# Optimization experiments

Measured on AMD Instinct MI355X. Metric: run time of the kernel, lower is better.

## Reference

```python
import jax, jax.numpy as jnp
import numpy as np

B0, H0, W0 = 4, 64, 64
D_MODEL, D_STATE, D_CONV, EXPAND = 192, 16, 3, 2.0
D_INNER = int(EXPAND * D_MODEL)          # 384
DT_RANK = (D_MODEL + 1) // 2             # 96
K = 4
EPS = 1e-5


def setup_inputs() -> dict:
    key = jax.random.key(0)
    ks = jax.random.split(key, 10)
    x = jax.random.normal(ks[0], (B0, H0, W0, D_MODEL), dtype=jnp.float32)
    in_proj_w = jax.random.normal(ks[1], (2 * D_INNER, D_MODEL), jnp.float32) * (D_MODEL ** -0.5)
    conv_w = jax.random.normal(ks[2], (D_INNER, 1, D_CONV, D_CONV), jnp.float32) * (1.0 / D_CONV)
    conv_b = jnp.zeros((D_INNER,), jnp.float32)
    x_proj_weight = jax.random.normal(ks[3], (K, DT_RANK + 2 * D_STATE, D_INNER), jnp.float32) * (D_INNER ** -0.5)
    dt_init_std = DT_RANK ** -0.5
    dt_projs_weight = jax.random.uniform(ks[4], (K, D_INNER, DT_RANK), jnp.float32, -dt_init_std, dt_init_std)
    # inverse-softplus init of dt bias, dt ~ loguniform[1e-3, 0.1]
    u = jax.random.uniform(ks[5], (K, D_INNER), jnp.float32)
    dt = jnp.exp(u * (np.log(0.1) - np.log(0.001)) + np.log(0.001))
    dt = jnp.clip(dt, 1e-4, None)
    dt_projs_bias = dt + jnp.log(-jnp.expm1(-dt))
    A_logs = jnp.log(jnp.tile(jnp.arange(1, D_STATE + 1, dtype=jnp.float32)[None, :], (K * D_INNER, 1)))
    Ds = jnp.ones((K * D_INNER,), jnp.float32)
    ln_gamma = jnp.ones((D_INNER,), jnp.float32)
    ln_beta = jnp.zeros((D_INNER,), jnp.float32)
    out_proj_w = jax.random.normal(ks[6], (D_MODEL, D_INNER), jnp.float32) * (D_INNER ** -0.5)
    return dict(x=x, in_proj_w=in_proj_w, conv_w=conv_w, conv_b=conv_b,
                x_proj_weight=x_proj_weight, dt_projs_weight=dt_projs_weight,
                dt_projs_bias=dt_projs_bias, A_logs=A_logs, Ds=Ds,
                ln_gamma=ln_gamma, ln_beta=ln_beta, out_proj_w=out_proj_w)


def _selective_scan(u, delta, A, Bs, Cs, Dp):
    # u, delta: (B,K,D,L); A: (K,D,N); Bs, Cs: (B,K,N,L); Dp: (K,D)
    b = u.shape[0]
    uT = jnp.transpose(u, (3, 0, 1, 2))      # (L,B,K,D)
    dT = jnp.transpose(delta, (3, 0, 1, 2))  # (L,B,K,D)
    BT = jnp.transpose(Bs, (3, 0, 1, 2))     # (L,B,K,N)
    CT = jnp.transpose(Cs, (3, 0, 1, 2))     # (L,B,K,N)
    h0 = jnp.zeros((b, K, D_INNER, D_STATE), u.dtype)

    def step(h, inp):
        dl, ul, Bl, Cl = inp
        dA = jnp.exp(dl[..., None] * A)                      # (B,K,D,N)
        h = dA * h + (dl * ul)[..., None] * Bl[:, :, None, :]  # (B,K,D,N)
        y = jnp.einsum('bkdn,bkn->bkd', h, Cl)
        return h, y

    _, ys = jax.lax.scan(step, h0, (dT, uT, BT, CT))
    y = jnp.transpose(ys, (1, 2, 3, 0))       # (B,K,D,L)
    return y + u * Dp[None, :, :, None]


def reference(x, in_proj_w, conv_w, conv_b, x_proj_weight, dt_projs_weight,
              dt_projs_bias, A_logs, Ds, ln_gamma, ln_beta, out_proj_w):
    B, H, W, C = x.shape
    L = H * W
    xz = jnp.einsum('bhwc,dc->bhwd', x, in_proj_w)           # (B,H,W,2*Di)
    xp, z = jnp.split(xz, 2, axis=-1)
    xc = jnp.transpose(xp, (0, 3, 1, 2))                      # (B,Di,H,W)
    xc = jax.lax.conv_general_dilated(
        xc, conv_w, window_strides=(1, 1), padding='SAME',
        feature_group_count=D_INNER,
        dimension_numbers=('NCHW', 'OIHW', 'NCHW')) + conv_b[None, :, None, None]
    xc = jax.nn.silu(xc)

    # cross-scan: 4 traversal orders
    x_flat = xc.reshape(B, D_INNER, L)
    x_wh = jnp.transpose(xc, (0, 1, 3, 2)).reshape(B, D_INNER, L)
    x_hwwh = jnp.stack([x_flat, x_wh], axis=1)                # (B,2,Di,L)
    xs = jnp.concatenate([x_hwwh, jnp.flip(x_hwwh, axis=-1)], axis=1)  # (B,4,Di,L)

    x_dbl = jnp.einsum('bkdl,kcd->bkcl', xs, x_proj_weight)
    dts = x_dbl[:, :, :DT_RANK]
    Bs = x_dbl[:, :, DT_RANK:DT_RANK + D_STATE]
    Cs = x_dbl[:, :, DT_RANK + D_STATE:]
    dts = jnp.einsum('bkrl,kdr->bkdl', dts, dt_projs_weight)
    delta = jax.nn.softplus(dts + dt_projs_bias[None, :, :, None])

    A = -jnp.exp(A_logs).reshape(K, D_INNER, D_STATE)
    Dp = Ds.reshape(K, D_INNER)
    out_y = _selective_scan(xs, delta, A, Bs, Cs, Dp)         # (B,4,Di,L)

    y1 = out_y[:, 0]
    inv_y = jnp.flip(out_y[:, 2:4], axis=-1)
    y2 = inv_y[:, 0]
    y3 = jnp.transpose(out_y[:, 1].reshape(B, D_INNER, W, H), (0, 1, 3, 2)).reshape(B, D_INNER, L)
    y4 = jnp.transpose(inv_y[:, 1].reshape(B, D_INNER, W, H), (0, 1, 3, 2)).reshape(B, D_INNER, L)
    y = y1 + y2 + y3 + y4                                     # (B,Di,L)

    y = jnp.transpose(y, (0, 2, 1)).reshape(B, H, W, D_INNER)
    mu = jnp.mean(y, axis=-1, keepdims=True)
    var = jnp.mean(jnp.square(y - mu), axis=-1, keepdims=True)
    y = (y - mu) * jax.lax.rsqrt(var + EPS) * ln_gamma + ln_beta
    y = y * jax.nn.silu(z)
    return jnp.einsum('bhwd,cd->bhwc', y, out_proj_w)
```

## Files before the change

kernel.cpp:

```cpp
#include <hip/hip_runtime.h>
#include <cstdint>

#define NSTATE  16
#define NCH     128
#define CH      32

typedef short bf16x8 __attribute__((ext_vector_type(8)));
typedef float f32x4  __attribute__((ext_vector_type(4)));
typedef float f32x2  __attribute__((ext_vector_type(2)));

__device__ __forceinline__ float b2f(unsigned short u) {
    union { unsigned int i; float f; } v; v.i = ((unsigned int)u) << 16; return v.f;
}
__device__ __forceinline__ unsigned short f2b(float f) {
    union { float f; unsigned int i; } v; v.f = f;
    unsigned int r = v.i + 0x7FFFu + ((v.i >> 16) & 1u);
    return (unsigned short)(r >> 16);
}
__device__ __forceinline__ f32x2 b2f2(unsigned int w) {
    union { unsigned int i; float f; } lo, hi;
    lo.i = w << 16; hi.i = w & 0xFFFF0000u;
    f32x2 r; r.x = lo.f; r.y = hi.f; return r;
}
__device__ __forceinline__ unsigned int f2b2(f32x2 v) {
    return (unsigned int)f2b(v.x) | ((unsigned int)f2b(v.y) << 16);
}
__device__ __forceinline__ f32x2 fma2(f32x2 a, f32x2 b, f32x2 c) {
#if __has_builtin(__builtin_elementwise_fma)
    return __builtin_elementwise_fma(a, b, c);
#else
    f32x2 r; r.x = fmaf(a.x, b.x, c.x); r.y = fmaf(a.y, b.y, c.y); return r;
#endif
}
__device__ __forceinline__ float exp2_fast(float x) {
    return __builtin_amdgcn_exp2f(x);
}
__device__ __forceinline__ float softplus_fast(float v) {
    return fmaxf(v, 0.f) + __logf(1.f + __expf(-fabsf(v)));
}
__device__ __forceinline__ void gload16(const void* g, void* l) {
    __builtin_amdgcn_global_load_lds(
        (const __attribute__((address_space(1))) void*)g,
        (__attribute__((address_space(3))) void*)l, 16, 0, 0);
}

__device__ __forceinline__ int pmap(int k, int i) {
    int l = i;
    if (k & 2) l = 4095 - l;
    if (k & 1) l = ((l & 63) << 6) | (l >> 6);
    return l;
}

__device__ __forceinline__ void epowers2(f32x2 E, f32x2* a) {
    a[0] = E;
    a[1] = a[0] * a[0];
    a[2] = a[1] * a[0];
    a[3] = a[1] * a[1];
    a[4] = a[3] * a[0];
    a[5] = a[3] * a[1];
    a[6] = a[3] * a[2];
    a[7] = a[3] * a[3];
    a[8]  = a[7] * a[0];
    a[9]  = a[7] * a[1];
    a[10] = a[7] * a[2];
    a[11] = a[7] * a[3];
    a[12] = a[7] * a[4];
    a[13] = a[7] * a[5];
    a[14] = a[7] * a[6];
    a[15] = a[7] * a[7];
}

__global__ __launch_bounds__(256)
void cast5(const float* __restrict__ s0, const float* __restrict__ s1,
           const float* __restrict__ s2, const float* __restrict__ s3,
           const float* __restrict__ s4, unsigned short* __restrict__ dst,
           int o1, int o2, int o3, int o4, int total)
{
    int i = (blockIdx.x * 256 + threadIdx.x) * 4;
    if (i >= total) return;
    const float* s; int off;
    if (i < o1)      { s = s0; off = 0;  }
    else if (i < o2) { s = s1; off = o1; }
    else if (i < o3) { s = s2; off = o2; }
    else if (i < o4) { s = s3; off = o3; }
    else             { s = s4; off = o4; }
    float4 v = *(const float4*)(s + (i - off));
    unsigned short o[4] = { f2b(v.x), f2b(v.y), f2b(v.z), f2b(v.w) };
    *(uint2*)(dst + i) = *(const uint2*)o;
}

__global__ __launch_bounds__(384)
void weff_k(const float* __restrict__ dtw, const float* __restrict__ xpw,
            unsigned short* __restrict__ wallb)
{
    int k = blockIdx.x;
    int dblk = blockIdx.y;
    int dp = threadIdx.x;
    if (dblk < 48) {
        const float* xb = xpw + (size_t)k * 128 * 384;
        const float* db = dtw + ((size_t)k * 384 + dblk * 8) * 96;
        float acc[8];
#pragma unroll
        for (int j = 0; j < 8; ++j) acc[j] = 0.f;
        for (int r = 0; r < 96; ++r) {
            float xv = xb[(size_t)r * 384 + dp];
#pragma unroll
            for (int j = 0; j < 8; ++j) acc[j] = fmaf(db[(size_t)j * 96 + r], xv, acc[j]);
        }
#pragma unroll
        for (int j = 0; j < 8; ++j)
            wallb[((size_t)k * 512 + dblk * 8 + j) * 384 + dp] = f2b(acc[j]);
    } else if (dblk < 52) {
        int r0 = (dblk - 48) * 8;
#pragma unroll
        for (int j = 0; j < 8; ++j)
            wallb[((size_t)k * 512 + 384 + r0 + j) * 384 + dp] =
                f2b(xpw[((size_t)k * 128 + 96 + r0 + j) * 384 + dp]);
    } else {
        int r0 = 416 + (dblk - 52) * 8;
#pragma unroll
        for (int j = 0; j < 8; ++j)
            wallb[((size_t)k * 512 + r0 + j) * 384 + dp] = 0;
    }
}

template<int MAP, int EPI, int OUTBF>
__global__ __launch_bounds__(512)
void gemm_pk3(const unsigned short* __restrict__ A, const unsigned short* __restrict__ A2,
              const unsigned short* __restrict__ W, void* __restrict__ Cv,
              float* __restrict__ aux, const float* __restrict__ bias,
              int Kd, int lda, int ldc, int wstride)
{
    __shared__ unsigned short As[3 * 256 * 32];
    __shared__ unsigned short Ws[3 * 128 * 32];
    const int bm = blockIdx.y * 256;
    const int bn = blockIdx.x * 128;
    const int t = threadIdx.x;
    const int lane = t & 63;
    const int wv = t >> 6;
    const int wm = wv & 3;
    const int wn = wv >> 2;

    int kb = 0;
    if (wstride) kb = (bm >> 12) & 3;
    const unsigned short* Wb = W + (size_t)kb * wstride;

    f32x4 acc[4][4];
#pragma unroll
    for (int i = 0; i < 4; ++i)
#pragma unroll
        for (int j = 0; j < 4; ++j) acc[i][j] = (f32x4){0.f, 0.f, 0.f, 0.f};

    const int cs = (t & 3) ^ ((t >> 3) & 3);
    const unsigned short* agsrc[2];
#pragma unroll
    for (int j = 0; j < 2; ++j) {
        int chunk = j * 512 + t;
        int row = chunk >> 2;
        size_t ro;
        if (MAP == 0) {
            ro = (size_t)(bm + row) * lda;
        } else {
            int r = bm + row;
            int bk = r >> 12, ii = r & 4095;
            int k = bk & 3, b = bk >> 2;
            int l = (k & 2) ? 4095 - ii : ii;
            const unsigned short* src = (k & 1) ? A2 : A;
            ro = (src - A) + ((size_t)b * 4096 + l) * 384;
        }
        agsrc[j] = A + ro + cs * 8;
    }
    const unsigned short* wgsrc = Wb + (size_t)(bn + (t >> 2)) * Kd + cs * 8;

    const int lr = lane & 15;
    const int chq = ((lane >> 4) ^ ((lane >> 1) & 3)) * 8;
    const int NT = Kd >> 5;

    auto stage = [&](int kt2, int buf) {
        const int k0 = kt2 << 5;
        char* asb = (char*)As + buf * 16384 + wv * 1024;
        char* wsb = (char*)Ws + buf * 8192 + wv * 1024;
        gload16(agsrc[0] + k0, asb);
        gload16(agsrc[1] + k0, asb + 8192);
        gload16(wgsrc + k0, wsb);
    };

    stage(0, 0);
    stage(1, 1);

    for (int kt = 0; kt < NT; ++kt) {
        if (kt == NT - 1) {
            asm volatile("s_waitcnt vmcnt(0)" ::: "memory");
        } else {
            asm volatile("s_waitcnt vmcnt(3)" ::: "memory");
        }
        __builtin_amdgcn_sched_barrier(0);
        __builtin_amdgcn_s_barrier();
        __builtin_amdgcn_sched_barrier(0);
        if (kt + 2 < NT) stage(kt + 2, (kt + 2) % 3);

        const unsigned short* Ab = As + (kt % 3) * (256 * 32);
        const unsigned short* Wt = Ws + (kt % 3) * (128 * 32);
        bf16x8 af[4], bfr[4];
#pragma unroll
        for (int mf = 0; mf < 4; ++mf)
            af[mf] = *(const bf16x8*)&Ab[(wm * 64 + mf * 16 + lr) * 32 + chq];
#pragma unroll
        for (int nf = 0; nf < 4; ++nf)
            bfr[nf] = *(const bf16x8*)&Wt[(wn * 64 + nf * 16 + lr) * 32 + chq];
#pragma unroll
        for (int mf = 0; mf < 4; ++mf)
#pragma unroll
            for (int nf = 0; nf < 4; ++nf)
                acc[mf][nf] = __builtin_amdgcn_mfma_f32_16x16x32_bf16(af[mf], bfr[nf], acc[mf][nf], 0, 0, 0);
    }

    const int lq = lane >> 4;
#pragma unroll
    for (int mf = 0; mf < 4; ++mf) {
#pragma unroll
        for (int nf = 0; nf < 4; ++nf) {
#pragma unroll
            for (int r = 0; r < 4; ++r) {
                int grow = bm + wm * 64 + mf * 16 + lq * 4 + r;
                int gcol = bn + wn * 64 + nf * 16 + lr;
                float v = acc[mf][nf][r];
                if (EPI == 0) {
                    if (OUTBF) ((unsigned short*)Cv)[(size_t)grow * ldc + gcol] = f2b(v);
                    else       ((float*)Cv)[(size_t)grow * ldc + gcol] = v;
                } else {
                    unsigned cc = (unsigned)gcol;
                    if (cc < 384u) {
                        v += bias[kb * 384 + cc];
                        v = softplus_fast(v);
                        ((unsigned short*)Cv)[(size_t)grow * 384 + cc] = f2b(v);
                    } else if (cc < 416u) {
                        aux[(size_t)grow * 32 + (cc - 384u)] = v;
                    }
                }
            }
        }
    }
}

__global__ __launch_bounds__(384)
void conv_silu(const unsigned short* __restrict__ xzb, const float* __restrict__ cw,
               const float* __restrict__ cb, unsigned short* __restrict__ xcb,
               unsigned short* __restrict__ xcbT)
{
    int t = threadIdx.x;
    int sub = (t >= 192) ? 1 : 0;
    int dp = t - sub * 192;
    int d0 = dp * 2;
    int bidx = blockIdx.x * 2 + sub;
    int l = bidx & 4095;
    int h = l >> 6, w = l & 63;
    const unsigned short* base = xzb + (size_t)(bidx - l) * 768;
    f32x2 acc; acc.x = cb[d0]; acc.y = cb[d0 + 1];
#pragma unroll
    for (int dy = -1; dy <= 1; ++dy) {
        int hh = h + dy;
        if ((unsigned)hh >= 64u) continue;
#pragma unroll
        for (int dx = -1; dx <= 1; ++dx) {
            int ww = w + dx;
            if ((unsigned)ww >= 64u) continue;
            f32x2 xv = b2f2(*(const unsigned int*)&base[(size_t)(hh * 64 + ww) * 768 + d0]);
            int wi = (dy + 1) * 3 + (dx + 1);
            f32x2 wv2; wv2.x = cw[d0 * 9 + wi]; wv2.y = cw[(d0 + 1) * 9 + wi];
            acc = fma2(xv, wv2, acc);
        }
    }
    f32x2 sig;
    sig.x = 1.f / (1.f + __expf(-acc.x));
    sig.y = 1.f / (1.f + __expf(-acc.y));
    acc *= sig;
    unsigned int v = f2b2(acc);
    *(unsigned int*)&xcb[(size_t)bidx * 384 + d0] = v;
    *(unsigned int*)&xcbT[((size_t)(bidx - l) + (w * 64 + h)) * 384 + d0] = v;
}

__global__ __launch_bounds__(384)
void scan1(const unsigned short* __restrict__ delta, const unsigned short* __restrict__ xcb,
           const unsigned short* __restrict__ xcbT, const float* __restrict__ bcf,
           const float* __restrict__ A_logs, unsigned short* __restrict__ csth,
           float* __restrict__ csts)
{
    int bid = blockIdx.x;
    int cpair = bid & 63;
    int bk = bid >> 6;
    int k = bk & 3, b = bk >> 2;
    int t = threadIdx.x;
    int sub = (__builtin_amdgcn_readfirstlane(t) >= 192) ? 1 : 0;
    int dp = t - sub * 192;
    int d0 = dp * 2;
    int c = cpair * 2 + sub;
    int i0 = c * CH;

    f32x2 A0l2;
    A0l2.x = -__expf(A_logs[((size_t)(k * 384 + d0)) * 16]) * 1.44269504f;
    A0l2.y = -__expf(A_logs[((size_t)(k * 384 + d0 + 1)) * 16]) * 1.44269504f;

    f32x2 h[NSTATE];
#pragma unroll
    for (int n = 0; n < NSTATE; ++n) h[n] = (f32x2){0.f, 0.f};
    f32x2 S = (f32x2){0.f, 0.f};

    const float* bcp = bcf + ((size_t)bk * 4096 + i0) * 32;
    size_t drow = ((size_t)bk * 4096 + i0) * 384 + d0;
    const unsigned short* usrc = (k & 1) ? xcbT : xcb;
    long ustep = (k & 2) ? -384 : 384;
    size_t urow = ((size_t)b * 4096 + ((k & 2) ? 4095 - i0 : i0)) * 384 + d0;

    unsigned int dw = *(const unsigned int*)&delta[drow];
    unsigned int uw = *(const unsigned int*)&usrc[urow];

    for (int ii = 0; ii < CH; ++ii) {
        unsigned int dwn = 0, uwn = 0;
        if (ii + 1 < CH) {
            dwn = *(const unsigned int*)&delta[drow + (ii + 1) * 384];
            uwn = *(const unsigned int*)&usrc[urow + (long)(ii + 1) * ustep];
        }
        const f32x4* P = (const f32x4*)(bcp + ii * 32);
        f32x4 B0 = P[0], B1 = P[1], B2 = P[2], B3 = P[3];

        f32x2 dl = b2f2(dw), u = b2f2(uw);
        S += dl;
        f32x2 ex = dl * A0l2;
        f32x2 E; E.x = exp2_fast(ex.x); E.y = exp2_fast(ex.y);
        f32x2 du = dl * u;
        f32x2 a[NSTATE];
        epowers2(E, a);
        float Bs[NSTATE] = {B0.x,B0.y,B0.z,B0.w, B1.x,B1.y,B1.z,B1.w,
                            B2.x,B2.y,B2.z,B2.w, B3.x,B3.y,B3.z,B3.w};
#pragma unroll
        for (int n = 0; n < NSTATE; ++n)
            h[n] = fma2(a[n], h[n], du * (f32x2){Bs[n], Bs[n]});
        dw = dwn; uw = uwn;
    }
    size_t hb = ((size_t)(bk * NCH + c) * 16) * 384 + d0;
#pragma unroll
    for (int n = 0; n < NSTATE; ++n)
        *(unsigned int*)&csth[hb + (size_t)n * 384] = f2b2(h[n]);
    *(f32x2*)&csts[(size_t)(bk * NCH + c) * 384 + d0] = S;
}

__global__ __launch_bounds__(384)
void scan2(unsigned short* __restrict__ csth, const float* __restrict__ csts,
           const float* __restrict__ A_logs)
{
    int bk = blockIdx.x, n = blockIdx.y;
    int d = threadIdx.x;
    int k = bk & 3;
    float An = -__expf(A_logs[((size_t)(k * 384 + d)) * 16 + n]);
    float H = 0.f;
    size_t hb0 = ((size_t)(bk * NCH) * 16 + n) * 384 + d;
    size_t sb0 = (size_t)(bk * NCH) * 384 + d;
    float S  = csts[sb0];
    float hF = b2f(csth[hb0]);
    for (int c = 0; c < NCH; ++c) {
        float Sn = 0.f, hFn = 0.f;
        if (c + 1 < NCH) {
            Sn  = csts[sb0 + (size_t)(c + 1) * 384];
            hFn = b2f(csth[hb0 + (size_t)(c + 1) * 16 * 384]);
        }
        csth[hb0 + (size_t)c * 16 * 384] = f2b(H);
        H = __expf(An * S) * H + hF;
        S = Sn; hF = hFn;
    }
}

__global__ __launch_bounds__(384)
void scan3(const unsigned short* __restrict__ delta, const unsigned short* __restrict__ xcb,
           const unsigned short* __restrict__ xcbT, const float* __restrict__ bcf,
           const float* __restrict__ A_logs, const float* __restrict__ Ds,
           const unsigned short* __restrict__ csth, unsigned short* __restrict__ yb)
{
    int bid = blockIdx.x;
    int cpair = bid & 63;
    int bk = bid >> 6;
    int k = bk & 3, b = bk >> 2;
    int t = threadIdx.x;
    int sub = (__builtin_amdgcn_readfirstlane(t) >= 192) ? 1 : 0;
    int dp = t - sub * 192;
    int d0 = dp * 2;
    int c = cpair * 2 + sub;
    int i0 = c * CH;

    f32x2 A0l2;
    A0l2.x = -__expf(A_logs[((size_t)(k * 384 + d0)) * 16]) * 1.44269504f;
    A0l2.y = -__expf(A_logs[((size_t)(k * 384 + d0 + 1)) * 16]) * 1.44269504f;

    f32x2 h[NSTATE];
    size_t hb = ((size_t)(bk * NCH + c) * 16) * 384 + d0;
#pragma unroll
    for (int n = 0; n < NSTATE; ++n)
        h[n] = b2f2(*(const unsigned int*)&csth[hb + (size_t)n * 384]);
    f32x2 Dp; Dp.x = Ds[k * 384 + d0]; Dp.y = Ds[k * 384 + d0 + 1];

    const float* bcp = bcf + ((size_t)bk * 4096 + i0) * 32;
    size_t drow = ((size_t)bk * 4096 + i0) * 384 + d0;
    const unsigned short* usrc = (k & 1) ? xcbT : xcb;
    long ustep = (k & 2) ? -384 : 384;
    size_t urow = ((size_t)b * 4096 + ((k & 2) ? 4095 - i0 : i0)) * 384 + d0;
    long ystep = (long)((k & 1) ? 64 : 1) * ((k & 2) ? -1 : 1) * 384;
    size_t yrow = ((size_t)bk * 4096 + pmap(k, i0)) * 384 + d0;

    unsigned int dw = *(const unsigned int*)&delta[drow];
    unsigned int uw = *(const unsigned int*)&usrc[urow];

    for (int ii = 0; ii < CH; ++ii) {
        unsigned int dwn = 0, uwn = 0;
        if (ii + 1 < CH) {
            dwn = *(const unsigned int*)&delta[drow + (ii + 1) * 384];
            uwn = *(const unsigned int*)&usrc[urow + (long)(ii + 1) * ustep];
        }
        const f32x4* P = (const f32x4*)(bcp + ii * 32);
        f32x4 B0 = P[0], B1 = P[1], B2 = P[2], B3 = P[3];
        f32x4 C0 = P[4], C1 = P[5], C2 = P[6], C3 = P[7];

        f32x2 dl = b2f2(dw), u = b2f2(uw);
        f32x2 ex = dl * A0l2;
        f32x2 E; E.x = exp2_fast(ex.x); E.y = exp2_fast(ex.y);
        f32x2 du = dl * u;
        f32x2 a[NSTATE];
        epowers2(E, a);
        float Bs[NSTATE] = {B0.x,B0.y,B0.z,B0.w, B1.x,B1.y,B1.z,B1.w,
                            B2.x,B2.y,B2.z,B2.w, B3.x,B3.y,B3.z,B3.w};
        float Cs[NSTATE] = {C0.x,C0.y,C0.z,C0.w, C1.x,C1.y,C1.z,C1.w,
                            C2.x,C2.y,C2.z,C2.w, C3.x,C3.y,C3.z,C3.w};
        f32x2 y = (f32x2){0.f, 0.f};
#pragma unroll
        for (int n = 0; n < NSTATE; ++n) {
            h[n] = fma2(a[n], h[n], du * (f32x2){Bs[n], Bs[n]});
            y = fma2(h[n], (f32x2){Cs[n], Cs[n]}, y);
        }
        y = fma2(u, Dp, y);
        *(unsigned int*)&yb[yrow + (long)ii * ystep] = f2b2(y);
        dw = dwn; uw = uwn;
    }
}

__global__ __launch_bounds__(384)
void combine_ln(const unsigned short* __restrict__ yb, const unsigned short* __restrict__ xzb,
                const float* __restrict__ gamma, const float* __restrict__ beta,
                unsigned short* __restrict__ ynb)
{
    int t = threadIdx.x;
    int sub = (t >= 192) ? 1 : 0;
    int dp = t - sub * 192;
    int d0 = dp * 2;
    int bid = blockIdx.x * 2 + sub;
    int b = bid >> 12, l = bid & 4095;
    size_t base = (((size_t)b * 4) * 4096 + l) * 384 + d0;
    f32x2 s = b2f2(*(const unsigned int*)&yb[base]);
    s += b2f2(*(const unsigned int*)&yb[base + (size_t)1 * 4096 * 384]);
    s += b2f2(*(const unsigned int*)&yb[base + (size_t)2 * 4096 * 384]);
    s += b2f2(*(const unsigned int*)&yb[base + (size_t)3 * 4096 * 384]);

    float s1 = s.x + s.y, s2 = s.x * s.x + s.y * s.y;
#pragma unroll
    for (int off = 32; off; off >>= 1) {
        s1 += __shfl_down(s1, off, 64);
        s2 += __shfl_down(s2, off, 64);
    }
    __shared__ float red[12];
    int wid = t >> 6;
    if ((t & 63) == 0) { red[wid] = s1; red[6 + wid] = s2; }
    __syncthreads();
    int wb = sub * 3;
    float sum   = red[wb] + red[wb + 1] + red[wb + 2];
    float sumsq = red[6 + wb] + red[6 + wb + 1] + red[6 + wb + 2];
    float mu  = sum * (1.f / 384.f);
    float var = sumsq * (1.f / 384.f) - mu * mu;
    float inv = rsqrtf(var + 1e-5f);
    f32x2 g2; g2.x = gamma[d0]; g2.y = gamma[d0 + 1];
    f32x2 b2; b2.x = beta[d0];  b2.y = beta[d0 + 1];
    f32x2 v = (s - mu) * inv * g2 + b2;
    f32x2 z = b2f2(*(const unsigned int*)&xzb[(size_t)bid * 768 + 384 + d0]);
    f32x2 sil; sil.x = z.x / (1.f + __expf(-z.x)); sil.y = z.y / (1.f + __expf(-z.y));
    v *= sil;
    *(unsigned int*)&ynb[(size_t)bid * 384 + d0] = f2b2(v);
}

__global__ __launch_bounds__(256)
void gemm_out(const unsigned short* __restrict__ A, const unsigned short* __restrict__ W,
              float* __restrict__ C, int Kd, int lda, int ldc)
{
    __shared__ unsigned short As[128 * 40];
    __shared__ unsigned short Ws[64 * 40];
    const int bm = blockIdx.x * 128;
    const int bn = blockIdx.y * 64;
    const int t = threadIdx.x;
    const int lane = t & 63;
    const int wv = t >> 6;
    const int wm = wv & 1;
    const int wn = wv >> 1;

    f32x4 acc[4][2];
#pragma unroll
    for (int i = 0; i < 4; ++i)
#pragma unroll
        for (int j = 0; j < 2; ++j) acc[i][j] = (f32x4){0.f, 0.f, 0.f, 0.f};

    size_t abase[2];
    int alw[2];
#pragma unroll
    for (int i = 0; i < 2; ++i) {
        int idx = i * 256 + t;
        int row = idx >> 2, c = idx & 3;
        alw[i] = row * 40 + c * 8;
        abase[i] = (size_t)(bm + row) * lda + c * 8;
    }
    const int wrow = t >> 2, wcol = t & 3;
    const size_t wbase = (size_t)(bn + wrow) * Kd + wcol * 8;
    const int wlw = wrow * 40 + wcol * 8;

    for (int k0 = 0; k0 < Kd; k0 += 32) {
        uint4 av0 = *(const uint4*)(A + abase[0] + k0);
        uint4 av1 = *(const uint4*)(A + abase[1] + k0);
        uint4 wv4 = *(const uint4*)(W + wbase + k0);
        __syncthreads();
        *(uint4*)&As[alw[0]] = av0;
        *(uint4*)&As[alw[1]] = av1;
        *(uint4*)&Ws[wlw] = wv4;
        __syncthreads();

        bf16x8 af[4], bfr[2];
        const int lr = lane & 15, lk = (lane >> 4) * 8;
#pragma unroll
        for (int mf = 0; mf < 4; ++mf)
            af[mf] = *(const bf16x8*)&As[(wm * 64 + mf * 16 + lr) * 40 + lk];
#pragma unroll
        for (int nf = 0; nf < 2; ++nf)
            bfr[nf] = *(const bf16x8*)&Ws[(wn * 32 + nf * 16 + lr) * 40 + lk];
#pragma unroll
        for (int mf = 0; mf < 4; ++mf)
#pragma unroll
            for (int nf = 0; nf < 2; ++nf)
                acc[mf][nf] = __builtin_amdgcn_mfma_f32_16x16x32_bf16(af[mf], bfr[nf], acc[mf][nf], 0, 0, 0);
    }

    const int lr = lane & 15, lq = lane >> 4;
#pragma unroll
    for (int mf = 0; mf < 4; ++mf)
#pragma unroll
        for (int nf = 0; nf < 2; ++nf)
#pragma unroll
            for (int r = 0; r < 4; ++r) {
                int grow = bm + wm * 64 + mf * 16 + lq * 4 + r;
                int gcol = bn + wn * 32 + nf * 16 + lr;
                C[(size_t)grow * ldc + gcol] = acc[mf][nf][r];
            }
}

extern "C" void kernel_launch(void* const* d_in, const int* in_sizes, int n_in,
                              void* d_out, int out_size, void* d_ws, size_t ws_size,
                              hipStream_t stream)
{
    const float* x    = (const float*)d_in[0];
    const float* ipw  = (const float*)d_in[1];
    const float* cw   = (const float*)d_in[2];
    const float* cb   = (const float*)d_in[3];
    const float* xpw  = (const float*)d_in[4];
    const float* dtw  = (const float*)d_in[5];
    const float* dtb  = (const float*)d_in[6];
    const float* alog = (const float*)d_in[7];
    const float* Dsp  = (const float*)d_in[8];
    const float* g    = (const float*)d_in[9];
    const float* bta  = (const float*)d_in[10];
    const float* opw  = (const float*)d_in[11];
    float* out = (float*)d_out;

    char* ws = (char*)d_ws;
    size_t o = 0;
    auto alloc_us = [&](size_t n) { unsigned short* p = (unsigned short*)(ws + o); o += n * 2; return p; };
    auto alloc_f  = [&](size_t n) { float* p = (float*)(ws + o); o += n * 4; return p; };

    unsigned short* xb     = alloc_us((size_t)16384 * 192);
    unsigned short* ipwb   = alloc_us((size_t)768 * 192);
    unsigned short* xpwb   = alloc_us((size_t)4 * 128 * 384);
    unsigned short* dtwb   = alloc_us((size_t)4 * 384 * 96);
    unsigned short* opwb   = alloc_us((size_t)192 * 384);
    unsigned short* wallb  = alloc_us((size_t)4 * 512 * 384);
    unsigned short* xzb    = alloc_us((size_t)16384 * 768);
    unsigned short* xcb    = alloc_us((size_t)16384 * 384);
    unsigned short* xcbT   = alloc_us((size_t)16384 * 384);
    float*          bcf    = alloc_f ((size_t)65536 * 32);
    unsigned short* deltab = alloc_us((size_t)65536 * 384);
    unsigned short* yb     = alloc_us((size_t)65536 * 384);
    unsigned short* csth   = alloc_us((size_t)16 * NCH * 16 * 384);
    float*          csts   = alloc_f ((size_t)16 * NCH * 384);
    unsigned short* ynb    = alloc_us((size_t)16384 * 384);
    (void)xpwb; (void)dtwb;

    const int n0 = 16384 * 192, n1 = 768 * 192, n2 = 4 * 128 * 384, n3 = 4 * 384 * 96, n4 = 192 * 384;
    const int o1 = n0, o2 = o1 + n1, o3 = o2 + n2, o4 = o3 + n3, tot = o4 + n4;
    cast5<<<(tot / 4 + 255) / 256, 256, 0, stream>>>(x, ipw, xpw, dtw, opw, xb, o1, o2, o3, o4, tot);
    weff_k<<<dim3(4, 64), 384, 0, stream>>>(dtw, xpw, wallb);

    gemm_pk3<0, 0, 1><<<dim3(6, 64), 512, 0, stream>>>(xb, nullptr, ipwb, xzb, nullptr, nullptr, 192, 192, 768, 0);
    conv_silu<<<8192, 384, 0, stream>>>(xzb, cw, cb, xcb, xcbT);
    gemm_pk3<2, 2, 1><<<dim3(4, 256), 512, 0, stream>>>(xcb, xcbT, wallb, deltab, bcf, dtb, 384, 384, 0, 512 * 384);
    scan1<<<16 * (NCH / 2), 384, 0, stream>>>(deltab, xcb, xcbT, bcf, alog, csth, csts);
    scan2<<<dim3(16, 16), 384, 0, stream>>>(csth, csts, alog);
    scan3<<<16 * (NCH / 2), 384, 0, stream>>>(deltab, xcb, xcbT, bcf, alog, Dsp, csth, yb);
    combine_ln<<<8192, 384, 0, stream>>>(yb, xzb, g, bta, ynb);
    gemm_out<<<dim3(128, 3), 256, 0, stream>>>(ynb, opwb, out, 384, 384, 192);
}
```

Before: 293.4 us.

## Use smaller unpipelined GEMM tiles, double scan chunk count, prefetch B/C

Replaces the 256x128 triple-buffered GEMM with a 128x128 single-buffered tile kernel that uses 256 threads and synchronises twice per k-step, with the grid reordered to put M on x. Doubles the number of scan chunks while halving chunk length, for more parallelism in scan1 and scan3. The scan loops also now prefetch the next step's B/C vectors. The GEMM loses its load/compute overlap, and the larger chunk count makes the scan2 chunk-state pass and its state buffers larger.

```diff
diff --git a/kernel.cpp b/kernel.cpp
--- a/kernel.cpp
+++ b/kernel.cpp
@@ -2,8 +2,8 @@
 #include <cstdint>
 
 #define NSTATE  16
-#define NCH     128
-#define CH      32
+#define NCH     256
+#define CH      16
 
 typedef short bf16x8 __attribute__((ext_vector_type(8)));
 typedef float f32x4  __attribute__((ext_vector_type(4)));
@@ -125,21 +125,21 @@
 }
 
 template<int MAP, int EPI, int OUTBF>
-__global__ __launch_bounds__(512)
-void gemm_pk3(const unsigned short* __restrict__ A, const unsigned short* __restrict__ A2,
-              const unsigned short* __restrict__ W, void* __restrict__ Cv,
-              float* __restrict__ aux, const float* __restrict__ bias,
-              int Kd, int lda, int ldc, int wstride)
-{
-    __shared__ unsigned short As[3 * 256 * 32];
-    __shared__ unsigned short Ws[3 * 128 * 32];
-    const int bm = blockIdx.y * 256;
-    const int bn = blockIdx.x * 128;
+__global__ __launch_bounds__(256)
+void gemm128(const unsigned short* __restrict__ A, const unsigned short* __restrict__ A2,
+             const unsigned short* __restrict__ W, void* __restrict__ Cv,
+             float* __restrict__ aux, const float* __restrict__ bias,
+             int Kd, int lda, int ldc, int wstride)
+{
+    __shared__ unsigned short As[128 * 32];
+    __shared__ unsigned short Ws[128 * 32];
+    const int bm = blockIdx.x * 128;
+    const int bn = blockIdx.y * 128;
     const int t = threadIdx.x;
     const int lane = t & 63;
     const int wv = t >> 6;
-    const int wm = wv & 3;
-    const int wn = wv >> 2;
+    const int wm = wv & 1;
+    const int wn = wv >> 1;
 
     int kb = 0;
     if (wstride) kb = (bm >> 12) & 3;
@@ -153,9 +153,10 @@
 
     const int cs = (t & 3) ^ ((t >> 3) & 3);
     const unsigned short* agsrc[2];
+    const unsigned short* wgsrc[2];
 #pragma unroll
     for (int j = 0; j < 2; ++j) {
-        int chunk = j * 512 + t;
+        int chunk = j * 256 + t;
         int row = chunk >> 2;
         size_t ro;
         if (MAP == 0) {
@@ -169,45 +170,29 @@
             ro = (src - A) + ((size_t)b * 4096 + l) * 384;
         }
         agsrc[j] = A + ro + cs * 8;
-    }
-    const unsigned short* wgsrc = Wb + (size_t)(bn + (t >> 2)) * Kd + cs * 8;
+        wgsrc[j] = Wb + (size_t)(bn + row) * Kd + cs * 8;
+    }
+    char* asb = (char*)As + wv * 1024;
+    char* wsb = (char*)Ws + wv * 1024;
 
     const int lr = lane & 15;
     const int chq = ((lane >> 4) ^ ((lane >> 1) & 3)) * 8;
-    const int NT = Kd >> 5;
-
-    auto stage = [&](int kt2, int buf) {
-        const int k0 = kt2 << 5;
-        char* asb = (char*)As + buf * 16384 + wv * 1024;
-        char* wsb = (char*)Ws + buf * 8192 + wv * 1024;
+
+    for (int k0 = 0; k0 < Kd; k0 += 32) {
+        __syncthreads();
         gload16(agsrc[0] + k0, asb);
-        gload16(agsrc[1] + k0, asb + 8192);
-        gload16(wgsrc + k0, wsb);
-    };
-
-    stage(0, 0);
-    stage(1, 1);
-
-    for (int kt = 0; kt < NT; ++kt) {
-        if (kt == NT - 1) {
-            asm volatile("s_waitcnt vmcnt(0)" ::: "memory");
-        } else {
-            asm volatile("s_waitcnt vmcnt(3)" ::: "memory");
-        }
-        __builtin_amdgcn_sched_barrier(0);
-        __builtin_amdgcn_s_barrier();
-        __builtin_amdgcn_sched_barrier(0);
-        if (kt + 2 < NT) stage(kt + 2, (kt + 2) % 3);
-
-        const unsigned short* Ab = As + (kt % 3) * (256 * 32);
-        const unsigned short* Wt = Ws + (kt % 3) * (128 * 32);
+        gload16(agsrc[1] + k0, asb + 4096);
+        gload16(wgsrc[0] + k0, wsb);
+        gload16(wgsrc[1] + k0, wsb + 4096);
+        __syncthreads();
+
         bf16x8 af[4], bfr[4];
 #pragma unroll
         for (int mf = 0; mf < 4; ++mf)
-            af[mf] = *(const bf16x8*)&Ab[(wm * 64 + mf * 16 + lr) * 32 + chq];
+            af[mf] = *(const bf16x8*)&As[(wm * 64 + mf * 16 + lr) * 32 + chq];
 #pragma unroll
         for (int nf = 0; nf < 4; ++nf)
-            bfr[nf] = *(const bf16x8*)&Wt[(wn * 64 + nf * 16 + lr) * 32 + chq];
+            bfr[nf] = *(const bf16x8*)&Ws[(wn * 64 + nf * 16 + lr) * 32 + chq];
 #pragma unroll
         for (int mf = 0; mf < 4; ++mf)
 #pragma unroll
@@ -228,6 +213,10 @@
                 if (EPI == 0) {
                     if (OUTBF) ((unsigned short*)Cv)[(size_t)grow * ldc + gcol] = f2b(v);
                     else       ((float*)Cv)[(size_t)grow * ldc + gcol] = v;
+                } else if (EPI == 1) {
+                    v += bias[kb * 384 + gcol];
+                    v = softplus_fast(v);
+                    ((unsigned short*)Cv)[(size_t)grow * ldc + gcol] = f2b(v);
                 } else {
                     unsigned cc = (unsigned)gcol;
                     if (cc < 384u) {
@@ -287,8 +276,8 @@
            float* __restrict__ csts)
 {
     int bid = blockIdx.x;
-    int cpair = bid & 63;
-    int bk = bid >> 6;
+    int cpair = bid & (NCH / 2 - 1);
+    int bk = bid / (NCH / 2);
     int k = bk & 3, b = bk >> 2;
     int t = threadIdx.x;
     int sub = (__builtin_amdgcn_readfirstlane(t) >= 192) ? 1 : 0;
@@ -314,15 +303,21 @@
 
     unsigned int dw = *(const unsigned int*)&delta[drow];
     unsigned int uw = *(const unsigned int*)&usrc[urow];
+    f32x4 B0, B1, B2, B3;
+    {
+        const f32x4* P = (const f32x4*)bcp;
+        B0 = P[0]; B1 = P[1]; B2 = P[2]; B3 = P[3];
+    }
 
     for (int ii = 0; ii < CH; ++ii) {
         unsigned int dwn = 0, uwn = 0;
+        f32x4 Bn0, Bn1, Bn2, Bn3;
         if (ii + 1 < CH) {
             dwn = *(const unsigned int*)&delta[drow + (ii + 1) * 384];
             uwn = *(const unsigned int*)&usrc[urow + (long)(ii + 1) * ustep];
-        }
-        const f32x4* P = (const f32x4*)(bcp + ii * 32);
-        f32x4 B0 = P[0], B1 = P[1], B2 = P[2], B3 = P[3];
+            const f32x4* Pn = (const f32x4*)(bcp + (ii + 1) * 32);
+            Bn0 = Pn[0]; Bn1 = Pn[1]; Bn2 = Pn[2]; Bn3 = Pn[3];
+        }
 
         f32x2 dl = b2f2(dw), u = b2f2(uw);
         S += dl;
@@ -337,6 +332,7 @@
         for (int n = 0; n < NSTATE; ++n)
             h[n] = fma2(a[n], h[n], du * (f32x2){Bs[n], Bs[n]});
         dw = dwn; uw = uwn;
+        B0 = Bn0; B1 = Bn1; B2 = Bn2; B3 = Bn3;
     }
     size_t hb = ((size_t)(bk * NCH + c) * 16) * 384 + d0;
 #pragma unroll
@@ -377,8 +373,8 @@
            const unsigned short* __restrict__ csth, unsigned short* __restrict__ yb)
 {
     int bid = blockIdx.x;
-    int cpair = bid & 63;
-    int bk = bid >> 6;
+    int cpair = bid & (NCH / 2 - 1);
+    int bk = bid / (NCH / 2);
     int k = bk & 3, b = bk >> 2;
     int t = threadIdx.x;
     int sub = (__builtin_amdgcn_readfirstlane(t) >= 192) ? 1 : 0;
@@ -408,16 +404,23 @@
 
     unsigned int dw = *(const unsigned int*)&delta[drow];
     unsigned int uw = *(const unsigned int*)&usrc[urow];
+    f32x4 B0, B1, B2, B3, C0, C1, C2, C3;
+    {
+        const f32x4* P = (const f32x4*)bcp;
+        B0 = P[0]; B1 = P[1]; B2 = P[2]; B3 = P[3];
+        C0 = P[4]; C1 = P[5]; C2 = P[6]; C3 = P[7];
+    }
 
     for (int ii = 0; ii < CH; ++ii) {
         unsigned int dwn = 0, uwn = 0;
+        f32x4 Bn0, Bn1, Bn2, Bn3, Cn0, Cn1, Cn2, Cn3;
         if (ii + 1 < CH) {
             dwn = *(const unsigned int*)&delta[drow + (ii + 1) * 384];
             uwn = *(const unsigned int*)&usrc[urow + (long)(ii + 1) * ustep];
-        }
-        const f32x4* P = (const f32x4*)(bcp + ii * 32);
-        f32x4 B0 = P[0], B1 = P[1], B2 = P[2], B3 = P[3];
-        f32x4 C0 = P[4], C1 = P[5], C2 = P[6], C3 = P[7];
+            const f32x4* Pn = (const f32x4*)(bcp + (ii + 1) * 32);
+            Bn0 = Pn[0]; Bn1 = Pn[1]; Bn2 = Pn[2]; Bn3 = Pn[3];
+            Cn0 = Pn[4]; Cn1 = Pn[5]; Cn2 = Pn[6]; Cn3 = Pn[7];
+        }
 
         f32x2 dl = b2f2(dw), u = b2f2(uw);
         f32x2 ex = dl * A0l2;
@@ -438,6 +441,8 @@
         y = fma2(u, Dp, y);
         *(unsigned int*)&yb[yrow + (long)ii * ystep] = f2b2(y);
         dw = dwn; uw = uwn;
+        B0 = Bn0; B1 = Bn1; B2 = Bn2; B3 = Bn3;
+        C0 = Cn0; C1 = Cn1; C2 = Cn2; C3 = Cn3;
     }
 }
 
@@ -599,9 +604,9 @@
     cast5<<<(tot / 4 + 255) / 256, 256, 0, stream>>>(x, ipw, xpw, dtw, opw, xb, o1, o2, o3, o4, tot);
     weff_k<<<dim3(4, 64), 384, 0, stream>>>(dtw, xpw, wallb);
 
-    gemm_pk3<0, 0, 1><<<dim3(6, 64), 512, 0, stream>>>(xb, nullptr, ipwb, xzb, nullptr, nullptr, 192, 192, 768, 0);
+    gemm128<0, 0, 1><<<dim3(128, 6), 256, 0, stream>>>(xb, nullptr, ipwb, xzb, nullptr, nullptr, 192, 192, 768, 0);
     conv_silu<<<8192, 384, 0, stream>>>(xzb, cw, cb, xcb, xcbT);
-    gemm_pk3<2, 2, 1><<<dim3(4, 256), 512, 0, stream>>>(xcb, xcbT, wallb, deltab, bcf, dtb, 384, 384, 0, 512 * 384);
+    gemm128<2, 2, 1><<<dim3(512, 4), 256, 0, stream>>>(xcb, xcbT, wallb, deltab, bcf, dtb, 384, 384, 384, 512 * 384);
     scan1<<<16 * (NCH / 2), 384, 0, stream>>>(deltab, xcb, xcbT, bcf, alog, csth, csts);
     scan2<<<dim3(16, 16), 384, 0, stream>>>(csth, csts, alog);
     scan3<<<16 * (NCH / 2), 384, 0, stream>>>(deltab, xcb, xcbT, bcf, alog, Dsp, csth, yb);
```

After: 320.1 us. +9.1%, slower.
